# Kernel tuning notes

Hardware: AMD Instinct MI355X
Metric: run time of the kernel (lower is better)

Reference implementation:

```python
import jax, jax.numpy as jnp
import numpy as np
from jax import lax

WORD_DIM = 300
VOCAB = 50000
PATTERN_LEN = 6
NUM_DIAGS = 3
DOC_LEN = 500000


def setup_inputs() -> dict:
    key = jax.random.key(0)
    k1, k2, k3, k4 = jax.random.split(key, 4)
    embeddings = jax.random.normal(k1, (WORD_DIM, VOCAB), dtype=jnp.float32)
    diags = jax.random.normal(k2, (NUM_DIAGS, WORD_DIM, PATTERN_LEN), dtype=jnp.float32)
    # original normalize(): each row (length pattern_length) of each diag divided by its norm
    diags = diags / jnp.linalg.norm(diags, axis=-1, keepdims=True)
    bias = jax.random.normal(k3, (NUM_DIAGS, PATTERN_LEN), dtype=jnp.float32)
    doc = jax.random.randint(k4, (DOC_LEN,), 0, VOCAB, dtype=jnp.int64)
    return {"embeddings": embeddings, "diags": diags, "bias": bias, "doc": doc}


def reference(embeddings, diags, bias, doc):
    P = diags.shape[-1]
    dtype = embeddings.dtype
    # Gather word vectors for the whole doc: (T, D)
    emb_doc = embeddings[:, doc].T
    # Only the "one forward" diagonal (index 1) is used by forward().
    # gate[t] = sigmoid(x_t @ diags[1] + bias[1])  -> (T, P)
    gate = jax.nn.sigmoid(jnp.einsum("td,dp->tp", emb_doc, diags[1]) + bias[1])
    start = jnp.zeros((P,), dtype=dtype).at[0].set(1.0)

    def step(carry, g):
        hidden, score = carry
        # hidden_new = start + [0, hidden[:-1] * gate[:-1]]
        shifted = jnp.concatenate([jnp.zeros((1,), dtype=dtype), hidden[:-1] * g[:-1]])
        hidden_new = start + shifted
        return (hidden_new, score + hidden_new[-1]), None

    (hidden, score), _ = lax.scan(step, (start, jnp.zeros((), dtype=dtype)), gate)
    return score
```

## Files before the change

kernel.cpp:

```cpp
#include <hip/hip_runtime.h>


#define WORD_DIM 300
#define VOCAB    50000
#define PLEN     6
#define DOC_LEN  500000

#define DSPLIT 10
#define DCHUNK 30

__global__ __launch_bounds__(256) void proj_partial_kernel(
    const float* __restrict__ emb,
    const float* __restrict__ diags,
    float* __restrict__ partial)
{
    __shared__ float wl[DCHUNK * 5];
    const int tid = threadIdx.x;
    const int c   = blockIdx.y;
    const int d0  = c * DCHUNK;
    for (int i = tid; i < DCHUNK * 5; i += 256) {
        int d = d0 + i / 5, p = i % 5;
        wl[i] = diags[WORD_DIM * PLEN + d * PLEN + p];
    }
    __syncthreads();

    const int v2 = (blockIdx.x * 256 + tid) * 2;
    if (v2 >= VOCAB) return;

    float ax[5] = {0.f, 0.f, 0.f, 0.f, 0.f};
    float ay[5] = {0.f, 0.f, 0.f, 0.f, 0.f};
    #pragma unroll
    for (int dd = 0; dd < DCHUNK; ++dd) {
        float2 x = *reinterpret_cast<const float2*>(&emb[(size_t)(d0 + dd) * VOCAB + v2]);
        #pragma unroll
        for (int p = 0; p < 5; ++p) {
            float w = wl[dd * 5 + p];
            ax[p] += x.x * w;
            ay[p] += x.y * w;
        }
    }
    #pragma unroll
    for (int p = 0; p < 5; ++p) {
        float2 o; o.x = ax[p]; o.y = ay[p];
        *reinterpret_cast<float2*>(&partial[(size_t)(p * DSPLIT + c) * VOCAB + v2]) = o;
    }
}

__global__ __launch_bounds__(256) void combine_sig_kernel(
    const float* __restrict__ partial,
    const float* __restrict__ bias,
    float* __restrict__ sig)
{
    const int v = blockIdx.x * 256 + threadIdx.x;
    if (v >= VOCAB) return;
    #pragma unroll
    for (int p = 0; p < 5; ++p) {
        float s = bias[PLEN + p];
        #pragma unroll
        for (int c = 0; c < DSPLIT; ++c)
            s += partial[(size_t)(p * DSPLIT + c) * VOCAB + v];
        sig[(size_t)v * 8 + p] = 1.f / (1.f + __expf(-s));
    }
}

#define K2_BLOCK 256
#define K2_TOK   (K2_BLOCK + 4)

__global__ __launch_bounds__(K2_BLOCK) void score_kernel(
    const int* __restrict__ doc,
    const float* __restrict__ sig,
    float* __restrict__ partials)
{
    __shared__ float srow[5][K2_TOK];
    const int tid  = threadIdx.x;
    const int base = blockIdx.x * K2_BLOCK + 4;
    for (int i = tid; i < K2_TOK; i += K2_BLOCK) {
        int tok_t = base - 4 + i;
        if (tok_t < DOC_LEN) {
            const float* row = &sig[(size_t)doc[tok_t] * 8];
            float4 r4 = *reinterpret_cast<const float4*>(row);
            srow[0][i] = r4.x; srow[1][i] = r4.y; srow[2][i] = r4.z; srow[3][i] = r4.w;
            srow[4][i] = row[4];
        }
    }
    __syncthreads();

    const int t = base + tid;
    float prod = 0.f;
    if (t < DOC_LEN) {
        prod = srow[0][tid] * srow[1][tid + 1] * srow[2][tid + 2]
             * srow[3][tid + 3] * srow[4][tid + 4];
    }
    #pragma unroll
    for (int off = 32; off > 0; off >>= 1)
        prod += __shfl_down(prod, off, 64);
    __shared__ float wsum[K2_BLOCK / 64];
    const int lane = tid & 63;
    const int wid  = tid >> 6;
    if (lane == 0) wsum[wid] = prod;
    __syncthreads();
    if (tid == 0) {
        float s = 0.f;
        #pragma unroll
        for (int w = 0; w < K2_BLOCK / 64; ++w) s += wsum[w];
        partials[blockIdx.x] = s;
    }
}

__global__ __launch_bounds__(256) void reduce_kernel(
    const float* __restrict__ partials, int n, float* __restrict__ out)
{
    float s = 0.f;
    for (int i = threadIdx.x; i < n; i += 256) s += partials[i];
    #pragma unroll
    for (int off = 32; off > 0; off >>= 1)
        s += __shfl_down(s, off, 64);
    __shared__ float wsum[4];
    const int lane = threadIdx.x & 63;
    const int wid  = threadIdx.x >> 6;
    if (lane == 0) wsum[wid] = s;
    __syncthreads();
    if (threadIdx.x == 0) out[0] = wsum[0] + wsum[1] + wsum[2] + wsum[3];
}

extern "C" void kernel_launch(void* const* d_in, const int* in_sizes, int n_in,
                              void* d_out, int out_size, void* d_ws, size_t ws_size,
                              hipStream_t stream) {
    const float* emb   = (const float*)d_in[0];
    const float* diags = (const float*)d_in[1];
    const float* bias  = (const float*)d_in[2];
    const int*   doc   = (const int*)d_in[3];
    float* out = (float*)d_out;

    float* ws = (float*)d_ws;
    float* sig     = ws;
    float* partial = sig + (size_t)VOCAB * 8;
    float* bpart   = partial + (size_t)5 * DSPLIT * VOCAB;

    const int blocks1 = (VOCAB / 2 + 255) / 256;
    const int blocksC = (VOCAB + 255) / 256;
    const int nwin    = DOC_LEN - 4;
    const int blocks2 = (nwin + K2_BLOCK - 1) / K2_BLOCK;

    dim3 g1(blocks1, DSPLIT);
    proj_partial_kernel<<<g1, 256, 0, stream>>>(emb, diags, partial);
    combine_sig_kernel<<<blocksC, 256, 0, stream>>>(partial, bias, sig);
    score_kernel<<<blocks2, K2_BLOCK, 0, stream>>>(doc, sig, bpart);
    reduce_kernel<<<1, 256, 0, stream>>>(bpart, blocks2, out);
}
```

Measured before the change: 29.94 us.

## Fuse projection and sigmoid via in-block split-D reduction, enlarge score blocks

The two-pass projection (partial sums per D-chunk written to global, then a combine+sigmoid kernel) is replaced by one kernel in which six thread groups each handle a 50-wide D chunk for the same 256 vocab columns and reduce their partials through shared memory before applying bias and sigmoid. This removes the 10M-float partial buffer round trip and one launch. The score kernel block grows to 1024 threads and the final reduce uses 512 threads to handle fewer partials. The cost is fewer, larger blocks for the projection (about 196 blocks of 768 threads), which may reduce occupancy and latency hiding on the strided embedding reads.

```diff
diff --git a/kernel.cpp b/kernel.cpp
--- a/kernel.cpp
+++ b/kernel.cpp
@@ -6,64 +6,69 @@
 #define PLEN     6
 #define DOC_LEN  500000
 
-#define DSPLIT 10
-#define DCHUNK 30
+#define GROUPS   6
+#define GSIZE    128
+#define DCHUNK   50
+#define K1_BLOCK (GROUPS * GSIZE)
 
-__global__ __launch_bounds__(256) void proj_partial_kernel(
+__global__ __launch_bounds__(K1_BLOCK) void proj_sig_fused(
     const float* __restrict__ emb,
     const float* __restrict__ diags,
-    float* __restrict__ partial)
+    const float* __restrict__ bias,
+    float* __restrict__ sig)
 {
-    __shared__ float wl[DCHUNK * 5];
+    __shared__ float wl[WORD_DIM * 5];
+    __shared__ float part[GROUPS - 1][GSIZE][10];
     const int tid = threadIdx.x;
-    const int c   = blockIdx.y;
-    const int d0  = c * DCHUNK;
-    for (int i = tid; i < DCHUNK * 5; i += 256) {
-        int d = d0 + i / 5, p = i % 5;
+    for (int i = tid; i < WORD_DIM * 5; i += K1_BLOCK) {
+        int d = i / 5, p = i % 5;
         wl[i] = diags[WORD_DIM * PLEN + d * PLEN + p];
     }
     __syncthreads();
 
-    const int v2 = (blockIdx.x * 256 + tid) * 2;
-    if (v2 >= VOCAB) return;
+    const int g  = tid / GSIZE;
+    const int u  = tid % GSIZE;
+    const int v2 = blockIdx.x * (2 * GSIZE) + u * 2;
+    const int d0 = g * DCHUNK;
 
-    float ax[5] = {0.f, 0.f, 0.f, 0.f, 0.f};
-    float ay[5] = {0.f, 0.f, 0.f, 0.f, 0.f};
-    #pragma unroll
-    for (int dd = 0; dd < DCHUNK; ++dd) {
-        float2 x = *reinterpret_cast<const float2*>(&emb[(size_t)(d0 + dd) * VOCAB + v2]);
+    float a[10] = {0.f, 0.f, 0.f, 0.f, 0.f, 0.f, 0.f, 0.f, 0.f, 0.f};
+    if (v2 < VOCAB) {
+        const float* __restrict__ col = emb + (size_t)d0 * VOCAB + v2;
+        #pragma unroll 10
+        for (int dd = 0; dd < DCHUNK; ++dd) {
+            float2 x = *reinterpret_cast<const float2*>(&col[(size_t)dd * VOCAB]);
+            const float* w = &wl[(d0 + dd) * 5];
+            a[0] += x.x * w[0]; a[1] += x.x * w[1]; a[2] += x.x * w[2];
+            a[3] += x.x * w[3]; a[4] += x.x * w[4];
+            a[5] += x.y * w[0]; a[6] += x.y * w[1]; a[7] += x.y * w[2];
+            a[8] += x.y * w[3]; a[9] += x.y * w[4];
+        }
+    }
+    if (g > 0) {
+        #pragma unroll
+        for (int k = 0; k < 10; ++k) part[g - 1][u][k] = a[k];
+    }
+    __syncthreads();
+    if (g == 0 && v2 < VOCAB) {
+        #pragma unroll
+        for (int k = 0; k < 10; ++k) {
+            float s = a[k];
+            #pragma unroll
+            for (int q = 0; q < GROUPS - 1; ++q) s += part[q][u][k];
+            a[k] = s;
+        }
+        float* r0 = &sig[(size_t)v2 * 8];
+        float* r1 = &sig[(size_t)(v2 + 1) * 8];
         #pragma unroll
         for (int p = 0; p < 5; ++p) {
-            float w = wl[dd * 5 + p];
-            ax[p] += x.x * w;
-            ay[p] += x.y * w;
+            float b = bias[PLEN + p];
+            r0[p] = 1.f / (1.f + __expf(-(a[p]     + b)));
+            r1[p] = 1.f / (1.f + __expf(-(a[5 + p] + b)));
         }
-    }
-    #pragma unroll
-    for (int p = 0; p < 5; ++p) {
-        float2 o; o.x = ax[p]; o.y = ay[p];
-        *reinterpret_cast<float2*>(&partial[(size_t)(p * DSPLIT + c) * VOCAB + v2]) = o;
     }
 }
 
-__global__ __launch_bounds__(256) void combine_sig_kernel(
-    const float* __restrict__ partial,
-    const float* __restrict__ bias,
-    float* __restrict__ sig)
-{
-    const int v = blockIdx.x * 256 + threadIdx.x;
-    if (v >= VOCAB) return;
-    #pragma unroll
-    for (int p = 0; p < 5; ++p) {
-        float s = bias[PLEN + p];
-        #pragma unroll
-        for (int c = 0; c < DSPLIT; ++c)
-            s += partial[(size_t)(p * DSPLIT + c) * VOCAB + v];
-        sig[(size_t)v * 8 + p] = 1.f / (1.f + __expf(-s));
-    }
-}
-
-#define K2_BLOCK 256
+#define K2_BLOCK 1024
 #define K2_TOK   (K2_BLOCK + 4)
 
 __global__ __launch_bounds__(K2_BLOCK) void score_kernel(
@@ -107,20 +112,25 @@
     }
 }
 
-__global__ __launch_bounds__(256) void reduce_kernel(
+__global__ __launch_bounds__(512) void reduce_kernel(
     const float* __restrict__ partials, int n, float* __restrict__ out)
 {
     float s = 0.f;
-    for (int i = threadIdx.x; i < n; i += 256) s += partials[i];
+    for (int i = threadIdx.x; i < n; i += 512) s += partials[i];
     #pragma unroll
     for (int off = 32; off > 0; off >>= 1)
         s += __shfl_down(s, off, 64);
-    __shared__ float wsum[4];
+    __shared__ float wsum[8];
     const int lane = threadIdx.x & 63;
     const int wid  = threadIdx.x >> 6;
     if (lane == 0) wsum[wid] = s;
     __syncthreads();
-    if (threadIdx.x == 0) out[0] = wsum[0] + wsum[1] + wsum[2] + wsum[3];
+    if (threadIdx.x == 0) {
+        float t = 0.f;
+        #pragma unroll
+        for (int w = 0; w < 8; ++w) t += wsum[w];
+        out[0] = t;
+    }
 }
 
 extern "C" void kernel_launch(void* const* d_in, const int* in_sizes, int n_in,
@@ -133,18 +143,14 @@
     float* out = (float*)d_out;
 
     float* ws = (float*)d_ws;
-    float* sig     = ws;
-    float* partial = sig + (size_t)VOCAB * 8;
-    float* bpart   = partial + (size_t)5 * DSPLIT * VOCAB;
+    float* sig   = ws;
+    float* bpart = sig + (size_t)VOCAB * 8;
 
-    const int blocks1 = (VOCAB / 2 + 255) / 256;
-    const int blocksC = (VOCAB + 255) / 256;
+    const int blocks1 = (VOCAB + 2 * GSIZE - 1) / (2 * GSIZE);
     const int nwin    = DOC_LEN - 4;
     const int blocks2 = (nwin + K2_BLOCK - 1) / K2_BLOCK;
 
-    dim3 g1(blocks1, DSPLIT);
-    proj_partial_kernel<<<g1, 256, 0, stream>>>(emb, diags, partial);
-    combine_sig_kernel<<<blocksC, 256, 0, stream>>>(partial, bias, sig);
+    proj_sig_fused<<<blocks1, K1_BLOCK, 0, stream>>>(emb, diags, bias, sig);
     score_kernel<<<blocks2, K2_BLOCK, 0, stream>>>(doc, sig, bpart);
-    reduce_kernel<<<1, 256, 0, stream>>>(bpart, blocks2, out);
+    reduce_kernel<<<1, 512, 0, stream>>>(bpart, blocks2, out);
 }
```

After: 26.05 us. -13.0%, faster.
